# Kernel tuning notes

Measured on AMD Instinct MI355X. Metric: run time of the kernel, lower is better.

The kernel has to match this reference:

```python
import jax, jax.numpy as jnp
import numpy as np

B, SP, SS = 8, 800, 48
DP, DS, DC = 2048, 1024, 1024
H, KV, HD = 8, 1, 256
FP, FS = 16384, 4096
EPS = 1e-6
ROPE_THETA = 10000.0
MASK_VAL = -2.3819763e38


def _rms(x, eps=EPS):
    var = jnp.mean(jnp.square(x.astype(jnp.float32)), axis=-1, keepdims=True)
    return (x * jax.lax.rsqrt(var + eps)).astype(x.dtype)


def _gemma_norm(x, w):
    # Gemma RMSNorm: norm(x) * (1 + weight); gate is None
    return _rms(x) * (1.0 + w)


def _ada_norm(x, cond, w, b):
    # dense(cond) -> [scale | shift | gate]; normed*(1+scale)+shift
    mod = cond @ w.T + b                      # [B, 3*D]
    scale, shift, gate = jnp.split(mod, 3, axis=-1)
    scale, shift, gate = scale[:, None, :], shift[:, None, :], gate[:, None, :]
    return _rms(x) * (1.0 + scale) + shift, gate


def _rotate_half(x):
    x1, x2 = jnp.split(x, 2, axis=-1)
    return jnp.concatenate([-x2, x1], axis=-1)


def _rope(q, k, position_ids):
    inv_freq = 1.0 / (ROPE_THETA ** (jnp.arange(0, HD, 2, dtype=jnp.float32) / HD))
    freqs = position_ids.astype(jnp.float32)[:, :, None] * inv_freq[None, None, :]
    emb = jnp.concatenate([freqs, freqs], axis=-1)      # [B, N, HD]
    cos = jnp.cos(emb)[:, None].astype(q.dtype)          # [B, 1, N, HD]
    sin = jnp.sin(emb)[:, None].astype(q.dtype)
    return q * cos + _rotate_half(q) * sin, k * cos + _rotate_half(k) * sin


def _mlp(x, gate_w, up_w, down_w):
    # Gemma GeGLU: down(gelu_tanh(gate(x)) * up(x))
    return (jax.nn.gelu(x @ gate_w.T, approximate=True) * (x @ up_w.T)) @ down_w.T


def _heads(x, w, n):  # x:[B,S,D] w:[n*HD,D] -> [B,n,S,HD]
    b, s, _ = x.shape
    return (x @ w.T).reshape(b, s, n, HD).transpose(0, 2, 1, 3)


def _forward(prefix_x, suffix_x, cond,
             p_ln_w, p_q_w, p_k_w, p_v_w, p_o_w, p_post_ln_w, p_gate_w, p_up_w, p_down_w,
             s_ada1_w, s_ada1_b, s_q_w, s_k_w, s_v_w, s_o_w, s_ada2_w, s_ada2_b,
             s_gate_w, s_up_w, s_down_w, position_ids, attn_mask):
    # per-stream norm + QKV
    hp = _gemma_norm(prefix_x, p_ln_w)                 # prefix: plain RMSNorm, gate None
    hs, gate_s = _ada_norm(suffix_x, cond, s_ada1_w, s_ada1_b)
    q = jnp.concatenate([_heads(hp, p_q_w, H), _heads(hs, s_q_w, H)], axis=2)   # [B,H,N,HD]
    k = jnp.concatenate([_heads(hp, p_k_w, KV), _heads(hs, s_k_w, KV)], axis=2)  # [B,1,N,HD]
    v = jnp.concatenate([_heads(hp, p_v_w, KV), _heads(hs, s_v_w, KV)], axis=2)
    q, k = _rope(q, k, position_ids)
    # GQA: repeat single KV head to H
    k = jnp.broadcast_to(k, (B, H, k.shape[2], HD))
    v = jnp.broadcast_to(v, (B, H, v.shape[2], HD))
    scaling = HD ** -0.5
    scores = jnp.einsum('bhqd,bhkd->bhqk', q, k) * scaling
    scores = scores + jnp.where(attn_mask[:, None], 0.0, MASK_VAL).astype(scores.dtype)
    attn = jax.nn.softmax(scores.astype(jnp.float32), axis=-1).astype(q.dtype)
    out = jnp.einsum('bhqk,bhkd->bhqd', attn, v)
    out = out.transpose(0, 2, 1, 3).reshape(B, -1, H * HD)   # [B, N, H*HD]
    # split back into streams
    op, os = out[:, :SP], out[:, SP:]
    # prefix: plain residuals
    res_p = prefix_x + op @ p_o_w.T
    out_p = res_p + _mlp(_gemma_norm(res_p, p_post_ln_w), p_gate_w, p_up_w, p_down_w)
    # suffix: gated residuals with AdaRMSNorm
    res_s = suffix_x + (os @ s_o_w.T) * gate_s
    h2, gate_s2 = _ada_norm(res_s, cond, s_ada2_w, s_ada2_b)
    out_s = res_s + _mlp(h2, s_gate_w, s_up_w, s_down_w) * gate_s2
    return out_p, out_s


def setup_inputs() -> dict:
    key = jax.random.key(0)
    ks = jax.random.split(key, 24)
    N = SP + SS
    std = 0.02
    d = {
        'prefix_x': jax.random.normal(ks[0], (B, SP, DP), jnp.float32),
        'suffix_x': jax.random.normal(ks[1], (B, SS, DS), jnp.float32),
        'cond': jax.random.normal(ks[2], (B, DC), jnp.float32),
        'p_ln_w': jax.random.normal(ks[3], (DP,), jnp.float32) * std,
        'p_q_w': jax.random.normal(ks[4], (H * HD, DP), jnp.float32) * std,
        'p_k_w': jax.random.normal(ks[5], (KV * HD, DP), jnp.float32) * std,
        'p_v_w': jax.random.normal(ks[6], (KV * HD, DP), jnp.float32) * std,
        'p_o_w': jax.random.normal(ks[7], (DP, H * HD), jnp.float32) * std,
        'p_post_ln_w': jax.random.normal(ks[8], (DP,), jnp.float32) * std,
        'p_gate_w': jax.random.normal(ks[9], (FP, DP), jnp.float32) * std,
        'p_up_w': jax.random.normal(ks[10], (FP, DP), jnp.float32) * std,
        'p_down_w': jax.random.normal(ks[11], (DP, FP), jnp.float32) * std,
        's_ada1_w': jax.random.normal(ks[12], (3 * DS, DC), jnp.float32) * std,
        's_ada1_b': jax.random.normal(ks[13], (3 * DS,), jnp.float32) * std,
        's_q_w': jax.random.normal(ks[14], (H * HD, DS), jnp.float32) * std,
        's_k_w': jax.random.normal(ks[15], (KV * HD, DS), jnp.float32) * std,
        's_v_w': jax.random.normal(ks[16], (KV * HD, DS), jnp.float32) * std,
        's_o_w': jax.random.normal(ks[17], (DS, H * HD), jnp.float32) * std,
        's_ada2_w': jax.random.normal(ks[18], (3 * DS, DC), jnp.float32) * std,
        's_ada2_b': jax.random.normal(ks[19], (3 * DS,), jnp.float32) * std,
        's_gate_w': jax.random.normal(ks[20], (FS, DS), jnp.float32) * std,
        's_up_w': jax.random.normal(ks[21], (FS, DS), jnp.float32) * std,
        's_down_w': jax.random.normal(ks[22], (DS, FS), jnp.float32) * std,
        'position_ids': jnp.broadcast_to(jnp.arange(N, dtype=jnp.int32), (B, N)),
    }
    # openpi block mask: prefix attends prefix only; suffix attends everything
    m = jnp.ones((N, N), dtype=bool).at[:SP, SP:].set(False)
    d['attn_mask'] = jnp.broadcast_to(m, (B, N, N))
    return d


def reference(prefix_x, suffix_x, cond,
              p_ln_w, p_q_w, p_k_w, p_v_w, p_o_w, p_post_ln_w, p_gate_w, p_up_w, p_down_w,
              s_ada1_w, s_ada1_b, s_q_w, s_k_w, s_v_w, s_o_w, s_ada2_w, s_ada2_b,
              s_gate_w, s_up_w, s_down_w, position_ids, attn_mask):
    return _forward(prefix_x, suffix_x, cond,
                    p_ln_w, p_q_w, p_k_w, p_v_w, p_o_w, p_post_ln_w, p_gate_w, p_up_w, p_down_w,
                    s_ada1_w, s_ada1_b, s_q_w, s_k_w, s_v_w, s_o_w, s_ada2_w, s_ada2_b,
                    s_gate_w, s_up_w, s_down_w, position_ids, attn_mask)
```

## Files before the change

### kernel.cpp

```cpp
#include <hip/hip_runtime.h>
#include <hip/hip_bf16.h>
#include <cmath>

using bf16 = __hip_bfloat16;
typedef short bf16x8 __attribute__((ext_vector_type(8)));
typedef float f32x4 __attribute__((ext_vector_type(4)));

#define GLD_LDS16(g, l) __builtin_amdgcn_global_load_lds( \
    (const __attribute__((address_space(1))) void*)(g),   \
    (__attribute__((address_space(3))) void*)(l), 16, 0, 0)

#define MFMA16(a,b,c) __builtin_amdgcn_mfma_f32_16x16x32_bf16((a),(b),(c),0,0,0)

#define C_SP 800
#define C_SS 48
#define C_B  8
#define C_N  848
#define C_NP 864
#define C_DP 2048
#define C_DS 1024
#define C_H  8
#define C_HD 256
#define C_FP 16384
#define C_FS 4096

__device__ inline float wredsum(float v){
  #pragma unroll
  for (int o = 32; o > 0; o >>= 1) v += __shfl_down(v, o, 64);
  return v;
}
__device__ inline float wredmax(float v){
  #pragma unroll
  for (int o = 32; o > 0; o >>= 1) v = fmaxf(v, __shfl_down(v, o, 64));
  return v;
}

__device__ inline void tile_swizzle(int lin, int nmt, int nnt, int& tm, int& tn){
  int total = nmt * nnt;
  int t;
  if ((total & 7) == 0) t = (lin & 7) * (total >> 3) + (lin >> 3);
  else t = lin;
  const int GN = 8;
  int band = GN * nmt;
  int g = t / band;
  int n0 = g * GN;
  int gw = nnt - n0; if (gw > GN) gw = GN;
  int r = t - g * band;
  tm = r / gw;
  tn = n0 + r % gw;
}

struct ConvTab {
  const float* src[14];
  bf16* dst[14];
  int cum[15];
};
__global__ void convert_all_k(ConvTab t){
  int b = blockIdx.x;
  int s = 0;
  #pragma unroll 1
  while (b >= t.cum[s+1]) ++s;
  long i = ((long)(b - t.cum[s]) * 256 + threadIdx.x) * 8;
  const float* src = t.src[s] + i;
  float4 v0 = *(const float4*)(src);
  float4 v1 = *(const float4*)(src + 4);
  bf16 o[8];
  o[0]=__float2bfloat16(v0.x); o[1]=__float2bfloat16(v0.y);
  o[2]=__float2bfloat16(v0.z); o[3]=__float2bfloat16(v0.w);
  o[4]=__float2bfloat16(v1.x); o[5]=__float2bfloat16(v1.y);
  o[6]=__float2bfloat16(v1.z); o[7]=__float2bfloat16(v1.w);
  *(int4*)(t.dst[s] + i) = *(const int4*)o;
}

__global__ void gemma_norm_k(const float* __restrict__ x, const float* __restrict__ w,
                             bf16* __restrict__ out){
  int row = blockIdx.x;
  int tid = threadIdx.x;
  const float* xr = x + (long)row * C_DP;
  float4 v0 = *(const float4*)(xr + tid*4);
  float4 v1 = *(const float4*)(xr + 1024 + tid*4);
  float ss = v0.x*v0.x + v0.y*v0.y + v0.z*v0.z + v0.w*v0.w
           + v1.x*v1.x + v1.y*v1.y + v1.z*v1.z + v1.w*v1.w;
  ss = wredsum(ss);
  __shared__ float red[4];
  if ((tid & 63) == 0) red[tid >> 6] = ss;
  __syncthreads();
  float tot = red[0] + red[1] + red[2] + red[3];
  float rs = rsqrtf(tot * (1.0f/2048.0f) + 1e-6f);
  bf16* orow = out + (long)row * C_DP;
  const float* wv = w;
  #pragma unroll
  for (int j = 0; j < 4; ++j){
    int c0 = tid*4 + j;
    orow[c0]        = __float2bfloat16(((&v0.x)[j]) * rs * (1.0f + wv[c0]));
    orow[c0 + 1024] = __float2bfloat16(((&v1.x)[j]) * rs * (1.0f + wv[c0 + 1024]));
  }
}

__global__ void ada_mod_k(const float* __restrict__ cond,
                          const float* __restrict__ w1, const float* __restrict__ b1,
                          const float* __restrict__ w2, const float* __restrict__ b2,
                          float* __restrict__ mod1, float* __restrict__ mod2){
  int idx = blockIdx.x * 256 + threadIdx.x;
  int sel = idx / 3072, col = idx - sel * 3072;
  const float* w = (sel ? w2 : w1) + (long)col * C_DS;
  float acc[8] = {0,0,0,0,0,0,0,0};
  for (int k = 0; k < C_DS; k += 4){
    float4 wv = *(const float4*)(w + k);
    #pragma unroll
    for (int b = 0; b < 8; ++b){
      float4 cv = *(const float4*)(cond + b*C_DS + k);
      acc[b] += wv.x*cv.x + wv.y*cv.y + wv.z*cv.z + wv.w*cv.w;
    }
  }
  float bias = (sel ? b2 : b1)[col];
  float* m = sel ? mod2 : mod1;
  #pragma unroll
  for (int b = 0; b < 8; ++b) m[b*3072 + col] = acc[b] + bias;
}

__global__ void ada_norm_k(const float* __restrict__ x, const float* __restrict__ mod,
                           bf16* __restrict__ out){
  int row = blockIdx.x;
  int b = row / C_SS;
  int tid = threadIdx.x;
  const float* xr = x + (long)row * C_DS;
  float4 v = *(const float4*)(xr + tid*4);
  float ss = v.x*v.x + v.y*v.y + v.z*v.z + v.w*v.w;
  ss = wredsum(ss);
  __shared__ float red[4];
  if ((tid & 63) == 0) red[tid >> 6] = ss;
  __syncthreads();
  float tot = red[0] + red[1] + red[2] + red[3];
  float rs = rsqrtf(tot * (1.0f/1024.0f) + 1e-6f);
  const float* mrow = mod + (long)b * 3072;
  bf16* orow = out + (long)row * C_DS;
  #pragma unroll
  for (int j = 0; j < 4; ++j){
    int col = tid*4 + j;
    float val = ((&v.x)[j]) * rs * (1.0f + mrow[col]) + mrow[1024 + col];
    orow[col] = __float2bfloat16(val);
  }
}

__global__ void rope_k(const float* __restrict__ qkv_p, const float* __restrict__ qkv_s,
                       bf16* __restrict__ q_r, bf16* __restrict__ k_r, bf16* __restrict__ v_t){
  int bn = blockIdx.x;
  int b = bn / C_N, n = bn - b * C_N;
  int d = threadIdx.x;
  const float* src = (n < C_SP) ? (qkv_p + ((long)b*C_SP + n) * 2560)
                                : (qkv_s + ((long)b*C_SS + (n - C_SP)) * 2560);
  int i = d & 127;
  float inv = expf(-(float)i * (9.210340371976184f / 128.0f));
  float fr = (float)n * inv;
  float sn, cs;
  sincosf(fr, &sn, &cs);
  bool lo = d < 128;
  int dpair = lo ? d + 128 : d - 128;
  #pragma unroll
  for (int h = 0; h < C_H; ++h){
    float a = src[h*C_HD + d], o = src[h*C_HD + dpair];
    float r = lo ? (a*cs - o*sn) : (a*cs + o*sn);
    q_r[(((long)b*C_H + h)*C_N + n)*C_HD + d] = __float2bfloat16(r);
  }
  {
    float a = src[2048 + d], o = src[2048 + dpair];
    float r = lo ? (a*cs - o*sn) : (a*cs + o*sn);
    k_r[((long)b*C_N + n)*C_HD + d] = __float2bfloat16(r);
  }
  v_t[((long)b*C_HD + d)*C_NP + n] = __float2bfloat16(src[2304 + d]);
  if (n < C_NP - C_N)
    v_t[((long)b*C_HD + d)*C_NP + C_N + n] = __float2bfloat16(0.0f);
}

__global__ void softmax_k(bf16* __restrict__ S){
  int m = blockIdx.x;
  int b = blockIdx.y;
  int qn = m % C_N;
  bf16* row = S + ((long)b * (C_H*C_N) + m) * C_NP;
  int tid = threadIdx.x, w = tid >> 6, lane = tid & 63;
  bool qpref = (qn < C_SP);
  float vals[4];
  float mx = -3.0e38f;
  #pragma unroll
  for (int j = 0; j < 4; ++j){
    int col = tid + j*256;
    float v = -3.0e38f;
    if (col < C_N && !(qpref && col >= C_SP)) v = __bfloat162float(row[col]);
    vals[j] = v; mx = fmaxf(mx, v);
  }
  mx = wredmax(mx);
  __shared__ float red[4];
  if (lane == 0) red[w] = mx;
  __syncthreads();
  mx = fmaxf(fmaxf(red[0], red[1]), fmaxf(red[2], red[3]));
  __syncthreads();
  float sum = 0.0f;
  #pragma unroll
  for (int j = 0; j < 4; ++j){
    float e = (vals[j] > -1.0e37f) ? __expf(vals[j] - mx) : 0.0f;
    vals[j] = e; sum += e;
  }
  sum = wredsum(sum);
  if (lane == 0) red[w] = sum;
  __syncthreads();
  sum = red[0] + red[1] + red[2] + red[3];
  float invs = 1.0f / sum;
  #pragma unroll
  for (int j = 0; j < 4; ++j){
    int col = tid + j*256;
    if (col < C_N) row[col] = __float2bfloat16(vals[j] * invs);
    else if (col < C_NP) row[col] = __float2bfloat16(0.0f);
  }
}

enum { M_F32 = 0, M_SBF16 = 1, M_ATTN_O = 2, M_RES_P = 3, M_RES_S = 4, M_OUT_P = 5, M_OUT_S = 6 };

template<int MODE>
__global__ __launch_bounds__(256, 2)
void gemm128(int nmt, int nnt,
             const bf16* __restrict__ Ab, long sA, int Ma,
             const bf16* __restrict__ Wb, long sW, int Nw,
             int K,
             void* __restrict__ Cb, long sC, int ldC, int Mc, int Nc,
             const float* __restrict__ aux0, long sAux0,
             const float* __restrict__ aux1,
             float scale)
{
  __shared__ bf16 As[128*32];
  __shared__ bf16 Bs[128*32];
  const int tid = threadIdx.x;
  const int w = tid >> 6, lane = tid & 63;
  const int wr = w >> 1, wc = w & 1;
  const int z = blockIdx.z;
  int tmi, tni;
  tile_swizzle(blockIdx.x, nmt, nnt, tmi, tni);
  const int tm = tmi * 128, tn = tni * 128;
  const bf16* A = Ab + (long)z * sA;
  const bf16* W = Wb + (long)z * sW;

  f32x4 acc[4][4] = {};

  const int r0 = tid >> 2;
  const int cb = (tid & 3) * 8;
  int ar0 = tm + r0;       if (ar0 >= Ma) ar0 = Ma - 1;
  int ar1 = tm + r0 + 64;  if (ar1 >= Ma) ar1 = Ma - 1;
  int nr0 = tn + r0;       if (nr0 >= Nw) nr0 = Nw - 1;
  int nr1 = tn + r0 + 64;  if (nr1 >= Nw) nr1 = Nw - 1;
  const bf16* ga0 = A + (long)ar0 * K + cb;
  const bf16* ga1 = A + (long)ar1 * K + cb;
  const bf16* gw0 = W + (long)nr0 * K + cb;
  const bf16* gw1 = W + (long)nr1 * K + cb;
  bf16* lA0 = As + tid * 8;
  bf16* lA1 = As + (tid + 256) * 8;
  bf16* lB0 = Bs + tid * 8;
  bf16* lB1 = Bs + (tid + 256) * 8;

  const int a_off = (wr*64 + (lane & 15)) * 32 + (lane >> 4) * 8;
  const int b_off = (wc*64 + (lane & 15)) * 32 + (lane >> 4) * 8;

  for (int kt = 0; kt < K; kt += 32){
    GLD_LDS16(ga0, lA0); GLD_LDS16(ga1, lA1);
    GLD_LDS16(gw0, lB0); GLD_LDS16(gw1, lB1);
    ga0 += 32; ga1 += 32; gw0 += 32; gw1 += 32;
    __syncthreads();
    bf16x8 af[4], bfr[4];
    #pragma unroll
    for (int r = 0; r < 4; ++r) af[r]  = *(const bf16x8*)(As + a_off + r*512);
    #pragma unroll
    for (int c = 0; c < 4; ++c) bfr[c] = *(const bf16x8*)(Bs + b_off + c*512);
    #pragma unroll
    for (int r = 0; r < 4; ++r)
      #pragma unroll
      for (int c = 0; c < 4; ++c)
        acc[r][c] = MFMA16(af[r], bfr[c], acc[r][c]);
    __syncthreads();
  }

  #pragma unroll
  for (int r = 0; r < 4; ++r){
    #pragma unroll
    for (int c = 0; c < 4; ++c){
      #pragma unroll
      for (int i = 0; i < 4; ++i){
        int row = tm + wr*64 + r*16 + (lane >> 4)*4 + i;
        int col = tn + wc*64 + c*16 + (lane & 15);
        if (row >= Mc || col >= Nc) continue;
        float v = acc[r][c][i];
        if constexpr (MODE == M_F32) {
          ((float*)Cb + (long)z*sC)[(long)row*ldC + col] = v;
        } else if constexpr (MODE == M_SBF16) {
          ((bf16*)Cb + (long)z*sC)[(long)row*ldC + col] = __float2bfloat16(v * scale);
        } else if constexpr (MODE == M_ATTN_O) {
          int h = row / C_N, qn = row - h*C_N;
          ((bf16*)Cb + (long)z*sC)[(long)qn*(C_H*C_HD) + h*C_HD + col] = __float2bfloat16(v);
        } else if constexpr (MODE == M_RES_P) {
          const float* X = aux0 + (long)z*sAux0;
          ((float*)Cb + (long)z*sC)[(long)row*ldC + col] = X[(long)row*ldC + col] + v;
        } else if constexpr (MODE == M_RES_S) {
          const float* X = aux0 + (long)z*sAux0;
          float g = aux1[z*3072 + 2048 + col];
          ((float*)Cb + (long)z*sC)[(long)row*ldC + col] = X[(long)row*ldC + col] + v * g;
        } else if constexpr (MODE == M_OUT_P) {
          ((float*)Cb)[(long)row*ldC + col] = aux0[(long)row*ldC + col] + v;
        } else if constexpr (MODE == M_OUT_S) {
          int bb = row / C_SS;
          ((float*)Cb)[(long)row*ldC + col] =
              aux0[(long)row*ldC + col] + v * aux1[bb*3072 + 2048 + col];
        }
      }
    }
  }
}

__global__ __launch_bounds__(256, 2)
void gemm_gateup(int nmt, int nnt,
                 const bf16* __restrict__ A, const bf16* __restrict__ Wg,
                 const bf16* __restrict__ Wu, int N, int K, bf16* __restrict__ act)
{
  __shared__ bf16 As[128*32];
  __shared__ bf16 Bg[64*32];
  __shared__ bf16 Bu[64*32];
  const int tid = threadIdx.x;
  const int w = tid >> 6, lane = tid & 63;
  const int wr = w >> 1, wc = w & 1;
  int tmi, tni;
  tile_swizzle(blockIdx.x, nmt, nnt, tmi, tni);
  const long tm = (long)tmi * 128;
  const int tn = tni * 64;

  f32x4 ag[4][2] = {}, au[4][2] = {};

  const int r0 = tid >> 2;
  const int cb = (tid & 3) * 8;
  const bf16* gA0 = A + (tm + r0) * K + cb;
  const bf16* gA1 = gA0 + (long)64 * K;
  const bf16* gG  = Wg + ((long)tn + r0) * K + cb;
  const bf16* gU  = Wu + ((long)tn + r0) * K + cb;
  bf16* lA0 = As + tid * 8;
  bf16* lA1 = As + (tid + 256) * 8;
  bf16* lG  = Bg + tid * 8;
  bf16* lU  = Bu + tid * 8;

  const int a_off = (wr*64 + (lane & 15)) * 32 + (lane >> 4) * 8;
  const int b_off = (wc*32 + (lane & 15)) * 32 + (lane >> 4) * 8;

  for (int kt = 0; kt < K; kt += 32){
    GLD_LDS16(gA0, lA0); GLD_LDS16(gA1, lA1);
    GLD_LDS16(gG, lG);   GLD_LDS16(gU, lU);
    gA0 += 32; gA1 += 32; gG += 32; gU += 32;
    __syncthreads();
    bf16x8 af[4], bg[2], bu[2];
    #pragma unroll
    for (int r = 0; r < 4; ++r) af[r] = *(const bf16x8*)(As + a_off + r*512);
    #pragma unroll
    for (int c = 0; c < 2; ++c){
      bg[c] = *(const bf16x8*)(Bg + b_off + c*512);
      bu[c] = *(const bf16x8*)(Bu + b_off + c*512);
    }
    #pragma unroll
    for (int r = 0; r < 4; ++r)
      #pragma unroll
      for (int c = 0; c < 2; ++c){
        ag[r][c] = MFMA16(af[r], bg[c], ag[r][c]);
        au[r][c] = MFMA16(af[r], bu[c], au[r][c]);
      }
    __syncthreads();
  }

  #pragma unroll
  for (int r = 0; r < 4; ++r)
    #pragma unroll
    for (int c = 0; c < 2; ++c)
      #pragma unroll
      for (int i = 0; i < 4; ++i){
        long row = tm + wr*64 + r*16 + (lane >> 4)*4 + i;
        int col = tn + wc*32 + c*16 + (lane & 15);
        float g = ag[r][c][i], u = au[r][c][i];
        float t = tanhf(0.7978845608f * (g + 0.044715f * g*g*g));
        act[row * N + col] = __float2bfloat16(0.5f * g * (1.0f + t) * u);
      }
}

extern "C" void kernel_launch(void* const* d_in, const int* in_sizes, int n_in,
                              void* d_out, int out_size, void* d_ws, size_t ws_size,
                              hipStream_t stream)
{
  (void)in_sizes; (void)n_in; (void)out_size; (void)ws_size;
  const float* prefix_x    = (const float*)d_in[0];
  const float* suffix_x    = (const float*)d_in[1];
  const float* cond        = (const float*)d_in[2];
  const float* p_ln_w      = (const float*)d_in[3];
  const float* p_q_w       = (const float*)d_in[4];
  const float* p_k_w       = (const float*)d_in[5];
  const float* p_v_w       = (const float*)d_in[6];
  const float* p_o_w       = (const float*)d_in[7];
  const float* p_post_ln_w = (const float*)d_in[8];
  const float* p_gate_w    = (const float*)d_in[9];
  const float* p_up_w      = (const float*)d_in[10];
  const float* p_down_w    = (const float*)d_in[11];
  const float* s_ada1_w    = (const float*)d_in[12];
  const float* s_ada1_b    = (const float*)d_in[13];
  const float* s_q_w       = (const float*)d_in[14];
  const float* s_k_w       = (const float*)d_in[15];
  const float* s_v_w       = (const float*)d_in[16];
  const float* s_o_w       = (const float*)d_in[17];
  const float* s_ada2_w    = (const float*)d_in[18];
  const float* s_ada2_b    = (const float*)d_in[19];
  const float* s_gate_w    = (const float*)d_in[20];
  const float* s_up_w      = (const float*)d_in[21];
  const float* s_down_w    = (const float*)d_in[22];

  char* ws = (char*)d_ws;
  size_t off = 0;
  auto alloc = [&](size_t b){ size_t o = off; off += (b + 255) & ~(size_t)255; return o; };

  size_t oWqkv_p = alloc((size_t)2560*2048*2);
  size_t oWqkv_s = alloc((size_t)2560*1024*2);
  size_t oWo_p   = alloc((size_t)2048*2048*2);
  size_t oWo_s   = alloc((size_t)1024*2048*2);
  size_t oWg_p   = alloc((size_t)16384*2048*2);
  size_t oWu_p   = alloc((size_t)16384*2048*2);
  size_t oWd_p   = alloc((size_t)2048*16384*2);
  size_t oWg_s   = alloc((size_t)4096*1024*2);
  size_t oWu_s   = alloc((size_t)4096*1024*2);
  size_t oWd_s   = alloc((size_t)1024*4096*2);
  size_t oHp   = alloc((size_t)6400*2048*2);
  size_t oHs   = alloc((size_t)384*1024*2);
  size_t oMod1 = alloc((size_t)8*3072*4);
  size_t oMod2 = alloc((size_t)8*3072*4);
  size_t oResS = alloc((size_t)384*1024*4);
  size_t oActS = alloc((size_t)384*4096*2);
  size_t oResP = alloc((size_t)6400*2048*4);
  size_t oQkvP = alloc((size_t)6400*2560*4);
  size_t oQkvS = alloc((size_t)384*2560*4);
  size_t oQr   = alloc((size_t)8*8*848*256*2);
  size_t oKr   = alloc((size_t)8*848*256*2);
  size_t oVt   = alloc((size_t)8*256*864*2);
  size_t oS    = alloc((size_t)8*6784*864*2);
  size_t oO    = alloc((size_t)8*848*2048*2);
  size_t oActP = oQkvP;

  {
    ConvTab t;
    struct { const float* s; size_t d; long n; } segs[14] = {
      {p_q_w,    oWqkv_p,                       (long)2048*2048},
      {p_k_w,    oWqkv_p + (size_t)2048*2048*2, (long)256*2048},
      {p_v_w,    oWqkv_p + (size_t)2304*2048*2, (long)256*2048},
      {s_q_w,    oWqkv_s,                       (long)2048*1024},
      {s_k_w,    oWqkv_s + (size_t)2048*1024*2, (long)256*1024},
      {s_v_w,    oWqkv_s + (size_t)2304*1024*2, (long)256*1024},
      {p_o_w,    oWo_p,   (long)2048*2048},
      {s_o_w,    oWo_s,   (long)1024*2048},
      {p_gate_w, oWg_p,   (long)16384*2048},
      {p_up_w,   oWu_p,   (long)16384*2048},
      {p_down_w, oWd_p,   (long)2048*16384},
      {s_gate_w, oWg_s,   (long)4096*1024},
      {s_up_w,   oWu_s,   (long)4096*1024},
      {s_down_w, oWd_s,   (long)1024*4096},
    };
    int c = 0;
    for (int i = 0; i < 14; ++i){
      t.src[i] = segs[i].s;
      t.dst[i] = (bf16*)(ws + segs[i].d);
      t.cum[i] = c;
      c += (int)(segs[i].n / 2048);
    }
    t.cum[14] = c;
    convert_all_k<<<c, 256, 0, stream>>>(t);
  }

  gemma_norm_k<<<6400, 256, 0, stream>>>(prefix_x, p_ln_w, (bf16*)(ws + oHp));
  ada_mod_k<<<24, 256, 0, stream>>>(cond, s_ada1_w, s_ada1_b, s_ada2_w, s_ada2_b,
                                    (float*)(ws + oMod1), (float*)(ws + oMod2));
  ada_norm_k<<<384, 256, 0, stream>>>(suffix_x, (const float*)(ws + oMod1), (bf16*)(ws + oHs));

  gemm128<M_F32><<<dim3(50*20,1,1), 256, 0, stream>>>(50, 20,
      (const bf16*)(ws+oHp), 0, 6400, (const bf16*)(ws+oWqkv_p), 0, 2560, 2048,
      ws+oQkvP, 0, 2560, 6400, 2560, nullptr, 0, nullptr, 1.0f);
  gemm128<M_F32><<<dim3(3*20,1,1), 256, 0, stream>>>(3, 20,
      (const bf16*)(ws+oHs), 0, 384, (const bf16*)(ws+oWqkv_s), 0, 2560, 1024,
      ws+oQkvS, 0, 2560, 384, 2560, nullptr, 0, nullptr, 1.0f);

  rope_k<<<8*848, 256, 0, stream>>>((const float*)(ws+oQkvP), (const float*)(ws+oQkvS),
                                    (bf16*)(ws+oQr), (bf16*)(ws+oKr), (bf16*)(ws+oVt));

  gemm128<M_SBF16><<<dim3(53*7,1,8), 256, 0, stream>>>(53, 7,
      (const bf16*)(ws+oQr), (long)6784*256, 6784,
      (const bf16*)(ws+oKr), (long)848*256, 848, 256,
      ws+oS, (long)6784*864, 864, 6784, 848, nullptr, 0, nullptr, 0.0625f);

  softmax_k<<<dim3(6784,8), 256, 0, stream>>>((bf16*)(ws+oS));

  gemm128<M_ATTN_O><<<dim3(53*2,1,8), 256, 0, stream>>>(53, 2,
      (const bf16*)(ws+oS), (long)6784*864, 6784,
      (const bf16*)(ws+oVt), (long)256*864, 256, 864,
      ws+oO, (long)848*2048, 2048, 6784, 256, nullptr, 0, nullptr, 1.0f);

  gemm128<M_RES_P><<<dim3(7*16,1,8), 256, 0, stream>>>(7, 16,
      (const bf16*)(ws+oO), (long)848*2048, 800,
      (const bf16*)(ws+oWo_p), 0, 2048, 2048,
      ws+oResP, (long)800*2048, 2048, 800, 2048, prefix_x, (long)800*2048, nullptr, 1.0f);
  gemm128<M_RES_S><<<dim3(1*8,1,8), 256, 0, stream>>>(1, 8,
      (const bf16*)(ws+oO) + (long)800*2048, (long)848*2048, 48,
      (const bf16*)(ws+oWo_s), 0, 1024, 2048,
      ws+oResS, (long)48*1024, 1024, 48, 1024, suffix_x, (long)48*1024,
      (const float*)(ws+oMod1), 1.0f);

  gemma_norm_k<<<6400, 256, 0, stream>>>((const float*)(ws+oResP), p_post_ln_w, (bf16*)(ws+oHp));
  ada_norm_k<<<384, 256, 0, stream>>>((const float*)(ws+oResS), (const float*)(ws+oMod2),
                                      (bf16*)(ws+oHs));

  gemm_gateup<<<dim3(50*256,1,1), 256, 0, stream>>>(50, 256,
      (const bf16*)(ws+oHp), (const bf16*)(ws+oWg_p), (const bf16*)(ws+oWu_p),
      16384, 2048, (bf16*)(ws+oActP));
  gemm128<M_OUT_P><<<dim3(50*16,1,1), 256, 0, stream>>>(50, 16,
      (const bf16*)(ws+oActP), 0, 6400, (const bf16*)(ws+oWd_p), 0, 2048, 16384,
      d_out, 0, 2048, 6400, 2048, (const float*)(ws+oResP), 0, nullptr, 1.0f);

  gemm_gateup<<<dim3(3*64,1,1), 256, 0, stream>>>(3, 64,
      (const bf16*)(ws+oHs), (const bf16*)(ws+oWg_s), (const bf16*)(ws+oWu_s),
      4096, 1024, (bf16*)(ws+oActS));
  gemm128<M_OUT_S><<<dim3(3*8,1,1), 256, 0, stream>>>(3, 8,
      (const bf16*)(ws+oActS), 0, 384, (const bf16*)(ws+oWd_s), 0, 1024, 4096,
      (float*)d_out + (size_t)6400*2048, 0, 1024, 384, 1024,
      (const float*)(ws+oResS), 0, (const float*)(ws+oMod2), 1.0f);
}
```

Baseline: 2.847 ms.

## Add 256x256-tile 8-wave GEMM with pipelined LDS staging for prefix GEMMs

Adds a new gemm256 kernel with 512 threads and 256x256 output tiles (256x128 per weight for gate/up). It uses double-buffered direct global-to-LDS loads interleaved with four MFMA quadrant phases and raises wave priority around the MFMA blocks. The kernel replaces the 128-tile kernels for the prefix QKV, gate/up and down projections, aiming to raise arithmetic intensity and overlap loads with compute. The trade-offs are 128KB of LDS per block and heavy register use, which limit occupancy. Fewer blocks (250 for QKV, 200 for down) may also underfill the CUs.

```diff
diff --git a/kernel.cpp b/kernel.cpp
--- a/kernel.cpp
+++ b/kernel.cpp
@@ -382,6 +382,152 @@
       }
 }
 
+enum { G_F32 = 0, G_OUT = 1, G_GU = 2 };
+
+#define G256_LDA(mh) \
+  _Pragma("unroll") for (int mf = 0; mf < 4; ++mf) \
+  _Pragma("unroll") for (int ks = 0; ks < 2; ++ks) \
+    aF[mf][ks] = *(const bf16x8*)(smem + D + (mh)*16384 + aoff + mf*2048 + ks*64);
+
+#define G256_LDB(nh) \
+  _Pragma("unroll") for (int nf = 0; nf < 2; ++nf) \
+  _Pragma("unroll") for (int ks = 0; ks < 2; ++ks) \
+    bF[nf][ks] = *(const bf16x8*)(smem + D + 32768 + (nh)*16384 + boff + nf*2048 + ks*64);
+
+#define G256_MM(mh, nh) \
+  __builtin_amdgcn_s_setprio(1); \
+  _Pragma("unroll") for (int mf = 0; mf < 4; ++mf) \
+  _Pragma("unroll") for (int nf = 0; nf < 2; ++nf) \
+  _Pragma("unroll") for (int ks = 0; ks < 2; ++ks) \
+    acc[mh][mf][nh][nf] = MFMA16(aF[mf][ks], bF[nf][ks], acc[mh][mf][nh][nf]); \
+  __builtin_amdgcn_s_setprio(0);
+
+#define G256_BAR __builtin_amdgcn_s_barrier()
+#define G256_LGKM0 asm volatile("s_waitcnt lgkmcnt(0)" ::: "memory")
+
+template<int MODE>
+__global__ __launch_bounds__(512, 2)
+void gemm256(int nmt, int nnt,
+             const bf16* __restrict__ A, int K,
+             const bf16* __restrict__ W0, const bf16* __restrict__ W1,
+             void* __restrict__ Cb, int ldC,
+             const float* __restrict__ aux0)
+{
+  __shared__ char smem[131072];
+  const int tid  = threadIdx.x;
+  const int lane = tid & 63;
+  const int w    = tid >> 6;
+  const int wr   = w >> 2;
+  const int wc   = w & 3;
+  const int NKT  = K >> 6;
+
+  int tmi, tni;
+  tile_swizzle(blockIdx.x, nmt, nnt, tmi, tni);
+  const int tm  = tmi * 256;
+  const int tn  = (MODE == G_GU) ? tni * 128 : tni * 256;
+  const int bn0 = tn;
+  const int bn1 = (MODE == G_GU) ? tn : tn + 128;
+
+  const int r0 = tid >> 3;
+  const int cg = (tid & 7) ^ (((tid >> 5) & 1) << 1);
+  const bf16* gA0 = A  + (size_t)(tm  + r0) * K + cg * 8;
+  const bf16* gA1 = gA0 + (size_t)128 * K;
+  const bf16* gB0 = W0 + (size_t)(bn0 + r0) * K + cg * 8;
+  const bf16* gB1 = W1 + (size_t)(bn1 + r0) * K + cg * 8;
+
+  auto STAGE = [&](const bf16* base, int ldsOff, int kt){
+    const bf16* s = base + (size_t)kt * 64;
+    char* d = smem + ldsOff + tid * 16;
+    GLD_LDS16(s, d);
+    GLD_LDS16(s + (size_t)64 * K, d + 8192);
+  };
+
+  const int koffswz = ((lane >> 4) * 16) ^ ((lane & 4) << 3);
+  const int aoff = (wr*64 + (lane & 15)) * 128 + koffswz;
+  const int boff = (wc*32 + (lane & 15)) * 128 + koffswz;
+
+  f32x4 acc[2][4][2][2] = {};
+  bf16x8 aF[4][2], bF[2][2];
+
+  STAGE(gA0, 0,         0);
+  STAGE(gB1, 49152,     0);
+  STAGE(gA1, 16384,     0);
+  STAGE(gB0, 32768,     0);
+  if (NKT > 1){
+    STAGE(gA0, 65536 + 0,     1);
+    STAGE(gB1, 65536 + 49152, 1);
+    STAGE(gA1, 65536 + 16384, 1);
+    asm volatile("s_waitcnt vmcnt(6)" ::: "memory");
+  } else {
+    asm volatile("s_waitcnt vmcnt(0)" ::: "memory");
+  }
+  G256_BAR;
+
+  for (int t = 0; t < NKT; ++t){
+    const int D  = (t & 1) << 16;
+    const int Dn = ((t + 1) & 1) << 16;
+    G256_LDA(0); G256_LDB(0);
+    if (t + 1 < NKT) STAGE(gB0, Dn + 32768, t + 1);
+    G256_BAR; G256_LGKM0;
+    G256_MM(0, 0);
+    G256_BAR;
+    G256_LDB(1);
+    if (t + 2 < NKT) STAGE(gA0, D + 0, t + 2);
+    G256_BAR; G256_LGKM0;
+    G256_MM(0, 1);
+    G256_BAR;
+    G256_LDA(1);
+    if (t + 2 < NKT) STAGE(gB1, D + 49152, t + 2);
+    G256_BAR; G256_LGKM0;
+    G256_MM(1, 1);
+    G256_BAR;
+    G256_LDB(0);
+    if (t + 2 < NKT) STAGE(gA1, D + 16384, t + 2);
+    G256_BAR; G256_LGKM0;
+    G256_MM(1, 0);
+    if (t < NKT - 2)       { asm volatile("s_waitcnt vmcnt(6)" ::: "memory"); }
+    else if (t == NKT - 2) { asm volatile("s_waitcnt vmcnt(0)" ::: "memory"); }
+    G256_BAR;
+  }
+
+  if constexpr (MODE == G_GU) {
+    bf16* act = (bf16*)Cb;
+    #pragma unroll
+    for (int mh = 0; mh < 2; ++mh)
+      #pragma unroll
+      for (int mf = 0; mf < 4; ++mf)
+        #pragma unroll
+        for (int nf = 0; nf < 2; ++nf)
+          #pragma unroll
+          for (int i = 0; i < 4; ++i){
+            long row = tm + mh*128 + wr*64 + mf*16 + (lane >> 4)*4 + i;
+            int  col = tn + wc*32 + nf*16 + (lane & 15);
+            float g = acc[mh][mf][0][nf][i];
+            float u = acc[mh][mf][1][nf][i];
+            float th = tanhf(0.7978845608f * (g + 0.044715f * g*g*g));
+            act[row * (long)ldC + col] = __float2bfloat16(0.5f * g * (1.0f + th) * u);
+          }
+  } else {
+    #pragma unroll
+    for (int mh = 0; mh < 2; ++mh)
+      #pragma unroll
+      for (int mf = 0; mf < 4; ++mf)
+        #pragma unroll
+        for (int nh = 0; nh < 2; ++nh)
+          #pragma unroll
+          for (int nf = 0; nf < 2; ++nf)
+            #pragma unroll
+            for (int i = 0; i < 4; ++i){
+              long row = tm + mh*128 + wr*64 + mf*16 + (lane >> 4)*4 + i;
+              int  col = tn + nh*128 + wc*32 + nf*16 + (lane & 15);
+              long idx = row * (long)ldC + col;
+              float v = acc[mh][mf][nh][nf][i];
+              if constexpr (MODE == G_F32) ((float*)Cb)[idx] = v;
+              else                         ((float*)Cb)[idx] = aux0[idx] + v;
+            }
+  }
+}
+
 extern "C" void kernel_launch(void* const* d_in, const int* in_sizes, int n_in,
                               void* d_out, int out_size, void* d_ws, size_t ws_size,
                               hipStream_t stream)
@@ -475,9 +621,10 @@
                                     (float*)(ws + oMod1), (float*)(ws + oMod2));
   ada_norm_k<<<384, 256, 0, stream>>>(suffix_x, (const float*)(ws + oMod1), (bf16*)(ws + oHs));
 
-  gemm128<M_F32><<<dim3(50*20,1,1), 256, 0, stream>>>(50, 20,
-      (const bf16*)(ws+oHp), 0, 6400, (const bf16*)(ws+oWqkv_p), 0, 2560, 2048,
-      ws+oQkvP, 0, 2560, 6400, 2560, nullptr, 0, nullptr, 1.0f);
+  gemm256<G_F32><<<dim3(25*10,1,1), 512, 0, stream>>>(25, 10,
+      (const bf16*)(ws+oHp), 2048,
+      (const bf16*)(ws+oWqkv_p), (const bf16*)(ws+oWqkv_p),
+      ws+oQkvP, 2560, nullptr);
   gemm128<M_F32><<<dim3(3*20,1,1), 256, 0, stream>>>(3, 20,
       (const bf16*)(ws+oHs), 0, 384, (const bf16*)(ws+oWqkv_s), 0, 2560, 1024,
       ws+oQkvS, 0, 2560, 384, 2560, nullptr, 0, nullptr, 1.0f);
@@ -511,12 +658,14 @@
   ada_norm_k<<<384, 256, 0, stream>>>((const float*)(ws+oResS), (const float*)(ws+oMod2),
                                       (bf16*)(ws+oHs));
 
-  gemm_gateup<<<dim3(50*256,1,1), 256, 0, stream>>>(50, 256,
-      (const bf16*)(ws+oHp), (const bf16*)(ws+oWg_p), (const bf16*)(ws+oWu_p),
-      16384, 2048, (bf16*)(ws+oActP));
-  gemm128<M_OUT_P><<<dim3(50*16,1,1), 256, 0, stream>>>(50, 16,
-      (const bf16*)(ws+oActP), 0, 6400, (const bf16*)(ws+oWd_p), 0, 2048, 16384,
-      d_out, 0, 2048, 6400, 2048, (const float*)(ws+oResP), 0, nullptr, 1.0f);
+  gemm256<G_GU><<<dim3(25*128,1,1), 512, 0, stream>>>(25, 128,
+      (const bf16*)(ws+oHp), 2048,
+      (const bf16*)(ws+oWg_p), (const bf16*)(ws+oWu_p),
+      ws+oActP, 16384, nullptr);
+  gemm256<G_OUT><<<dim3(25*8,1,1), 512, 0, stream>>>(25, 8,
+      (const bf16*)(ws+oActP), 16384,
+      (const bf16*)(ws+oWd_p), (const bf16*)(ws+oWd_p),
+      d_out, 2048, (const float*)(ws+oResP));
 
   gemm_gateup<<<dim3(3*64,1,1), 256, 0, stream>>>(3, 64,
       (const bf16*)(ws+oHs), (const bf16*)(ws+oWg_s), (const bf16*)(ws+oWu_s),
```

Measured after the change: 2.674 ms. 6.1% less time.
